# Performance work log

Measured on AMD Instinct MI355X. Metric: run time of the kernel, lower is better.

## Reference

```python
import jax, jax.numpy as jnp
import numpy as np

N_OSC = 32
CONV = 1000.0  # convergence_factor


def _cpg_ode(y, ia, ifr, cw, pb):
    # Faithful to CPGOde.forward, including its unpacking order:
    # (amplitudes, amplitudes_dot, phases) = (y[:n], y[n:2n], y[2n:3n])
    n = N_OSC
    a = y[:n]
    a_dot = y[n:2 * n]
    ph = y[2 * n:3 * n]
    phase_dots = ifr + jnp.sum(a[:, None] * cw * jnp.sin(ph[None, :] - ph[:, None] - pb), axis=1)
    a_dd = CONV * (CONV / 4.0 * (ia - a) - a_dot)
    # states_to_tensor(amplitudes_dot, phase_dots, amplitudes_dot_dot)
    return jnp.concatenate([a_dot, phase_dots, a_dd])


def _rk4_38_step(f, y, h):
    # torchdiffeq 'rk4' = rk4_alt_step_func (3/8 rule), one step over t=[0, h]
    k1 = f(y)
    k2 = f(y + h * k1 / 3.0)
    k3 = f(y + h * (k2 - k1 / 3.0))
    k4 = f(y + h * (k1 - k2 + k3))
    return y + h * 0.125 * (k1 + 3.0 * (k2 + k3) + k4)


def _mlp(x, Ws, bs):
    # Linear stack with ReLU between layers, none after the last
    for i, (W, b) in enumerate(zip(Ws, bs)):
        x = W @ x + b
        if i < len(Ws) - 1:
            x = jax.nn.relu(x)
    return x


def _init_linear(key, fan_in, fan_out):
    kW, kb = jax.random.split(key)
    bound = 1.0 / np.sqrt(fan_in)
    W = jax.random.uniform(kW, (fan_out, fan_in), minval=-bound, maxval=bound, dtype=jnp.float32)
    b = jax.random.uniform(kb, (fan_out,), minval=-bound, maxval=bound, dtype=jnp.float32)
    return W, b


def setup_inputs() -> dict:
    key = jax.random.key(0)
    ks = jax.random.split(key, 10)
    n = N_OSC
    n_params = 2 * n + 2 * n * n  # 2112
    in_dims = [2049, 4096, 4096, n_params]  # input_layers[0]+1, ..., final param layer
    out_dims = [2 * n, 2048, 2048, 1024]
    inp = {}
    inp["state"] = jax.random.normal(ks[0], (3 * n,), dtype=jnp.float32) * 0.1
    inp["x"] = jax.random.normal(ks[1], (2048,), dtype=jnp.float32)
    inp["timestep"] = jnp.array(0.01, dtype=jnp.float32)
    for i in range(3):
        W, b = _init_linear(ks[2 + i], in_dims[i], in_dims[i + 1])
        inp[f"in_W{i}"] = W
        inp[f"in_b{i}"] = b
    for i in range(3):
        W, b = _init_linear(ks[5 + i], out_dims[i], out_dims[i + 1])
        inp[f"out_W{i}"] = W
        inp[f"out_b{i}"] = b
    return inp


def reference(state, x, timestep,
              in_W0, in_b0, in_W1, in_b1, in_W2, in_b2,
              out_W0, out_b0, out_W1, out_b1, out_W2, out_b2):
    n = N_OSC
    # append timestep scalar to the input features
    x = jnp.concatenate([x, timestep[None]])
    params = _mlp(x, [in_W0, in_W1, in_W2], [in_b0, in_b1, in_b2])
    ia = params[:n]
    ifr = params[n:2 * n]
    cw = params[2 * n:2 * n + n * n].reshape(n, n)
    pb = params[2 * n + n * n:].reshape(n, n)
    f = lambda y: _cpg_ode(y, ia, ifr, cw, pb)
    new_state = _rk4_38_step(f, state, timestep)
    a = new_state[:n]
    ph = new_state[n:2 * n]
    cpg_out = jnp.concatenate([a * jnp.cos(ph), a * jnp.sin(ph)])
    out = _mlp(cpg_out, [out_W0, out_W1, out_W2], [out_b0, out_b1, out_b2])
    return (jax.lax.stop_gradient(new_state), out)
```

## Files before the change

kernel.cpp:

```cpp
#include <hip/hip_runtime.h>
#include <stdint.h>

template<int RELU, int TS>
__global__ __launch_bounds__(256) void gemv_k(
    const float* __restrict__ W, const float* __restrict__ B,
    const float* __restrict__ x, const float* __restrict__ ts,
    float* __restrict__ y, int cols)
{
    int tid = threadIdx.x;
    int row = blockIdx.x;
    int n = TS ? cols - 1 : cols;
    const float* w = W + (size_t)row * (size_t)cols;

    int mis = (int)(((uintptr_t)w >> 2) & 3);
    int start = (4 - mis) & 3;
    if (start > n) start = n;

    float sum = 0.0f;
    if (tid < start) sum += w[tid] * x[tid];

    int nv = (n - start) >> 2;
    const float4* wv = (const float4*)(w + start);
    const float* xs = x + start;

    int g = tid;
    for (; g + 768 < nv; g += 1024) {
        float4 u0 = wv[g];
        float4 u1 = wv[g + 256];
        float4 u2 = wv[g + 512];
        float4 u3 = wv[g + 768];
        const float* x0 = xs + 4 * g;
        const float* x1 = xs + 4 * (g + 256);
        const float* x2 = xs + 4 * (g + 512);
        const float* x3 = xs + 4 * (g + 768);
        sum += u0.x * x0[0] + u0.y * x0[1] + u0.z * x0[2] + u0.w * x0[3];
        sum += u1.x * x1[0] + u1.y * x1[1] + u1.z * x1[2] + u1.w * x1[3];
        sum += u2.x * x2[0] + u2.y * x2[1] + u2.z * x2[2] + u2.w * x2[3];
        sum += u3.x * x3[0] + u3.y * x3[1] + u3.z * x3[2] + u3.w * x3[3];
    }
    for (; g < nv; g += 256) {
        float4 u = wv[g];
        const float* xp = xs + 4 * g;
        sum += u.x * xp[0] + u.y * xp[1] + u.z * xp[2] + u.w * xp[3];
    }
    int t = start + nv * 4 + tid;
    if (t < n) sum += w[t] * x[t];
    if (TS && tid == 0) sum += w[n] * ts[0];

    #pragma unroll
    for (int off = 32; off > 0; off >>= 1) sum += __shfl_down(sum, off);
    __shared__ float red[4];
    if ((tid & 63) == 0) red[tid >> 6] = sum;
    __syncthreads();
    if (tid == 0) {
        float r = red[0] + red[1] + red[2] + red[3] + B[row];
        if (RELU) r = fmaxf(r, 0.0f);
        y[row] = r;
    }
}

__global__ __launch_bounds__(64) void ode_k(
    const float* __restrict__ state, const float* __restrict__ ts,
    const float* __restrict__ params, float* __restrict__ cpg,
    float* __restrict__ out_state)
{
    const float CONV = 1000.0f;
    __shared__ float s_cw[32 * 33];
    __shared__ float s_spb[32 * 33];
    __shared__ float s_cpb[32 * 33];
    __shared__ float s_s[32], s_c[32];
    int tid = threadIdx.x;

    for (int k = tid; k < 1024; k += 64) {
        int p = k + (k >> 5);
        s_cw[p] = params[64 + k];
        float pb = params[1088 + k];
        float sp, cp;
        sincosf(pb, &sp, &cp);
        s_spb[p] = sp;
        s_cpb[p] = cp;
    }
    __syncthreads();

    bool act = (tid < 32);
    int i = tid;
    float ia = 0.f, ifr = 0.f, y0a = 0.f, y0b = 0.f, y0c = 0.f;
    if (act) {
        ia  = params[i];
        ifr = params[32 + i];
        y0a = state[i];
        y0b = state[32 + i];
        y0c = state[64 + i];
    }
    float h = ts[0];

    float k1a=0,k1b=0,k1c=0, k2a=0,k2b=0,k2c=0, k3a=0,k3b=0,k3c=0, k4a=0,k4b=0,k4c=0;

    auto do_eval = [&](float a, float ad, float ph,
                       float& fa, float& fb, float& fc) {
        __syncthreads();
        if (act) {
            float s, c;
            sincosf(ph, &s, &c);
            s_s[i] = s; s_c[i] = c;
        }
        __syncthreads();
        if (act) {
            float si = s_s[i], ci = s_c[i];
            float ssum = 0.0f;
            #pragma unroll
            for (int j = 0; j < 32; j++) {
                float sj = s_s[j], cj = s_c[j];
                float sdp = sj * ci - cj * si;
                float cdp = cj * ci + sj * si;
                int p = i * 33 + j;
                float sv = sdp * s_cpb[p] - cdp * s_spb[p];
                ssum += s_cw[p] * sv;
            }
            fa = ad;
            fb = ifr + a * ssum;
            fc = CONV * (CONV * 0.25f * (ia - a) - ad);
        }
    };

    do_eval(y0a, y0b, y0c, k1a, k1b, k1c);
    do_eval(y0a + h * k1a / 3.0f,
            y0b + h * k1b / 3.0f,
            y0c + h * k1c / 3.0f, k2a, k2b, k2c);
    do_eval(y0a + h * (k2a - k1a / 3.0f),
            y0b + h * (k2b - k1b / 3.0f),
            y0c + h * (k2c - k1c / 3.0f), k3a, k3b, k3c);
    do_eval(y0a + h * (k1a - k2a + k3a),
            y0b + h * (k1b - k2b + k3b),
            y0c + h * (k1c - k2c + k3c), k4a, k4b, k4c);

    if (act) {
        float na = y0a + h * 0.125f * (k1a + 3.0f * (k2a + k3a) + k4a);
        float nb = y0b + h * 0.125f * (k1b + 3.0f * (k2b + k3b) + k4b);
        float nc = y0c + h * 0.125f * (k1c + 3.0f * (k2c + k3c) + k4c);
        out_state[i]      = na;
        out_state[32 + i] = nb;
        out_state[64 + i] = nc;
        cpg[i]      = na * cosf(nb);
        cpg[32 + i] = na * sinf(nb);
    }
}

extern "C" void kernel_launch(void* const* d_in, const int* in_sizes, int n_in,
                              void* d_out, int out_size, void* d_ws, size_t ws_size,
                              hipStream_t stream) {
    const float* state = (const float*)d_in[0];
    const float* x     = (const float*)d_in[1];
    const float* ts    = (const float*)d_in[2];
    const float* inW0  = (const float*)d_in[3];
    const float* inb0  = (const float*)d_in[4];
    const float* inW1  = (const float*)d_in[5];
    const float* inb1  = (const float*)d_in[6];
    const float* inW2  = (const float*)d_in[7];
    const float* inb2  = (const float*)d_in[8];
    const float* oW0   = (const float*)d_in[9];
    const float* ob0   = (const float*)d_in[10];
    const float* oW1   = (const float*)d_in[11];
    const float* ob1   = (const float*)d_in[12];
    const float* oW2   = (const float*)d_in[13];
    const float* ob2   = (const float*)d_in[14];

    float* ws  = (float*)d_ws;
    float* h0  = ws;
    float* h1  = ws + 4096;
    float* pr  = ws + 8192;
    float* cpg = ws + 10304;
    float* g0  = ws + 10368;
    float* g1  = ws + 12416;

    float* out = (float*)d_out;

    gemv_k<1,1><<<4096, 256, 0, stream>>>(inW0, inb0, x,   ts,      h0, 2049);
    gemv_k<1,0><<<4096, 256, 0, stream>>>(inW1, inb1, h0,  nullptr, h1, 4096);
    gemv_k<0,0><<<2112, 256, 0, stream>>>(inW2, inb2, h1,  nullptr, pr, 4096);
    ode_k<<<1, 64, 0, stream>>>(state, ts, pr, cpg, out);
    gemv_k<1,0><<<2048, 256, 0, stream>>>(oW0,  ob0,  cpg, nullptr, g0, 64);
    gemv_k<1,0><<<2048, 256, 0, stream>>>(oW1,  ob1,  g0,  nullptr, g1, 2048);
    gemv_k<0,0><<<1024, 256, 0, stream>>>(oW2,  ob2,  g1,  nullptr, out + 96, 2048);
}
```

Before: 214.1 us.

## Fuse all GEMV stages and ODE into one cooperative persistent kernel

Replaces the seven separate kernel launches with a single cooperative kernel of 1024 persistent blocks. Stages are separated by grid-wide syncs, and each block computes two rows per iteration. The ODE integrator now runs in block 0 with 256 threads. This removes launch gaps and tail idle between the small dependent stages, at the cost of grid.sync overhead, the loss of the 4-way unrolled load loop, and a fixed grid that may underfill the GPU during the bandwidth-bound large GEMVs.

```diff
diff --git a/kernel.cpp b/kernel.cpp
--- a/kernel.cpp
+++ b/kernel.cpp
@@ -1,82 +1,86 @@
 #include <hip/hip_runtime.h>
+#include <hip/hip_cooperative_groups.h>
 #include <stdint.h>
 
-template<int RELU, int TS>
-__global__ __launch_bounds__(256) void gemv_k(
-    const float* __restrict__ W, const float* __restrict__ B,
-    const float* __restrict__ x, const float* __restrict__ ts,
-    float* __restrict__ y, int cols)
-{
-    int tid = threadIdx.x;
-    int row = blockIdx.x;
-    int n = TS ? cols - 1 : cols;
-    const float* w = W + (size_t)row * (size_t)cols;
-
+namespace cg = cooperative_groups;
+
+#define NBLK 1024
+
+__device__ __forceinline__ float dot_row(const float* __restrict__ w,
+                                         const float* __restrict__ x,
+                                         int n, int tid)
+{
     int mis = (int)(((uintptr_t)w >> 2) & 3);
     int start = (4 - mis) & 3;
     if (start > n) start = n;
-
     float sum = 0.0f;
     if (tid < start) sum += w[tid] * x[tid];
-
     int nv = (n - start) >> 2;
     const float4* wv = (const float4*)(w + start);
     const float* xs = x + start;
-
-    int g = tid;
-    for (; g + 768 < nv; g += 1024) {
-        float4 u0 = wv[g];
-        float4 u1 = wv[g + 256];
-        float4 u2 = wv[g + 512];
-        float4 u3 = wv[g + 768];
-        const float* x0 = xs + 4 * g;
-        const float* x1 = xs + 4 * (g + 256);
-        const float* x2 = xs + 4 * (g + 512);
-        const float* x3 = xs + 4 * (g + 768);
-        sum += u0.x * x0[0] + u0.y * x0[1] + u0.z * x0[2] + u0.w * x0[3];
-        sum += u1.x * x1[0] + u1.y * x1[1] + u1.z * x1[2] + u1.w * x1[3];
-        sum += u2.x * x2[0] + u2.y * x2[1] + u2.z * x2[2] + u2.w * x2[3];
-        sum += u3.x * x3[0] + u3.y * x3[1] + u3.z * x3[2] + u3.w * x3[3];
-    }
-    for (; g < nv; g += 256) {
+    for (int g = tid; g < nv; g += 256) {
         float4 u = wv[g];
         const float* xp = xs + 4 * g;
         sum += u.x * xp[0] + u.y * xp[1] + u.z * xp[2] + u.w * xp[3];
     }
     int t = start + nv * 4 + tid;
     if (t < n) sum += w[t] * x[t];
-    if (TS && tid == 0) sum += w[n] * ts[0];
-
-    #pragma unroll
-    for (int off = 32; off > 0; off >>= 1) sum += __shfl_down(sum, off);
-    __shared__ float red[4];
-    if ((tid & 63) == 0) red[tid >> 6] = sum;
-    __syncthreads();
-    if (tid == 0) {
-        float r = red[0] + red[1] + red[2] + red[3] + B[row];
-        if (RELU) r = fmaxf(r, 0.0f);
-        y[row] = r;
-    }
-}
-
-__global__ __launch_bounds__(64) void ode_k(
-    const float* __restrict__ state, const float* __restrict__ ts,
-    const float* __restrict__ params, float* __restrict__ cpg,
-    float* __restrict__ out_state)
+    return sum;
+}
+
+template<int RELU, int TSCOL>
+__device__ void gemv_stage(const float* __restrict__ W, const float* __restrict__ B,
+                           const float* __restrict__ x, const float* __restrict__ ts,
+                           float* __restrict__ y, int rows, int cols,
+                           float* __restrict__ red)
+{
+    int tid = threadIdx.x;
+    int n = TSCOL ? cols - 1 : cols;
+    for (int base = blockIdx.x * 2; base < rows; base += NBLK * 2) {
+        int r1ok = (base + 1 < rows);
+        const float* w0 = W + (size_t)base * (size_t)cols;
+        const float* w1 = w0 + (r1ok ? cols : 0);
+        float s0 = dot_row(w0, x, n, tid);
+        float s1 = dot_row(w1, x, n, tid);
+        if (TSCOL && tid == 0) {
+            float t0 = ts[0];
+            s0 += w0[n] * t0;
+            s1 += w1[n] * t0;
+        }
+        #pragma unroll
+        for (int off = 32; off > 0; off >>= 1) {
+            s0 += __shfl_down(s0, off);
+            s1 += __shfl_down(s1, off);
+        }
+        __syncthreads();
+        if ((tid & 63) == 0) { red[tid >> 6] = s0; red[4 + (tid >> 6)] = s1; }
+        __syncthreads();
+        if (tid == 0) {
+            float r = red[0] + red[1] + red[2] + red[3] + B[base];
+            if (RELU) r = fmaxf(r, 0.0f);
+            y[base] = r;
+        } else if (tid == 64 && r1ok) {
+            float r = red[4] + red[5] + red[6] + red[7] + B[base + 1];
+            if (RELU) r = fmaxf(r, 0.0f);
+            y[base + 1] = r;
+        }
+    }
+}
+
+__device__ void ode_stage(const float* __restrict__ state, const float* __restrict__ ts,
+                          const float* __restrict__ params, float* __restrict__ cpg,
+                          float* __restrict__ out_state,
+                          float* s_cw, float* s_spb, float* s_cpb,
+                          float* s_s, float* s_c)
 {
     const float CONV = 1000.0f;
-    __shared__ float s_cw[32 * 33];
-    __shared__ float s_spb[32 * 33];
-    __shared__ float s_cpb[32 * 33];
-    __shared__ float s_s[32], s_c[32];
     int tid = threadIdx.x;
 
-    for (int k = tid; k < 1024; k += 64) {
+    for (int k = tid; k < 1024; k += 256) {
         int p = k + (k >> 5);
         s_cw[p] = params[64 + k];
-        float pb = params[1088 + k];
         float sp, cp;
-        sincosf(pb, &sp, &cp);
+        sincosf(params[1088 + k], &sp, &cp);
         s_spb[p] = sp;
         s_cpb[p] = cp;
     }
@@ -144,6 +148,45 @@
         cpg[i]      = na * cosf(nb);
         cpg[32 + i] = na * sinf(nb);
     }
+}
+
+__global__ __launch_bounds__(256, 4) void fused_k(
+    const float* state, const float* x, const float* ts,
+    const float* inW0, const float* inb0,
+    const float* inW1, const float* inb1,
+    const float* inW2, const float* inb2,
+    const float* oW0,  const float* ob0,
+    const float* oW1,  const float* ob1,
+    const float* oW2,  const float* ob2,
+    float* out, float* ws)
+{
+    cg::grid_group grid = cg::this_grid();
+
+    float* h0  = ws;
+    float* h1  = ws + 4096;
+    float* pr  = ws + 8192;
+    float* cpg = ws + 10304;
+    float* g0  = ws + 10368;
+    float* g1  = ws + 12416;
+
+    __shared__ float s_red[8];
+    __shared__ float s_cw[1056], s_spb[1056], s_cpb[1056];
+    __shared__ float s_s[32], s_c[32];
+
+    gemv_stage<1,1>(inW0, inb0, x,   ts, h0, 4096, 2049, s_red);
+    grid.sync();
+    gemv_stage<1,0>(inW1, inb1, h0,  nullptr, h1, 4096, 4096, s_red);
+    grid.sync();
+    gemv_stage<0,0>(inW2, inb2, h1,  nullptr, pr, 2112, 4096, s_red);
+    grid.sync();
+    if (blockIdx.x == 0)
+        ode_stage(state, ts, pr, cpg, out, s_cw, s_spb, s_cpb, s_s, s_c);
+    grid.sync();
+    gemv_stage<1,0>(oW0, ob0, cpg, nullptr, g0, 2048, 64, s_red);
+    grid.sync();
+    gemv_stage<1,0>(oW1, ob1, g0,  nullptr, g1, 2048, 2048, s_red);
+    grid.sync();
+    gemv_stage<0,0>(oW2, ob2, g1,  nullptr, out + 96, 1024, 2048, s_red);
 }
 
 extern "C" void kernel_launch(void* const* d_in, const int* in_sizes, int n_in,
@@ -165,21 +208,19 @@
     const float* oW2   = (const float*)d_in[13];
     const float* ob2   = (const float*)d_in[14];
 
+    float* out = (float*)d_out;
     float* ws  = (float*)d_ws;
-    float* h0  = ws;
-    float* h1  = ws + 4096;
-    float* pr  = ws + 8192;
-    float* cpg = ws + 10304;
-    float* g0  = ws + 10368;
-    float* g1  = ws + 12416;
-
-    float* out = (float*)d_out;
-
-    gemv_k<1,1><<<4096, 256, 0, stream>>>(inW0, inb0, x,   ts,      h0, 2049);
-    gemv_k<1,0><<<4096, 256, 0, stream>>>(inW1, inb1, h0,  nullptr, h1, 4096);
-    gemv_k<0,0><<<2112, 256, 0, stream>>>(inW2, inb2, h1,  nullptr, pr, 4096);
-    ode_k<<<1, 64, 0, stream>>>(state, ts, pr, cpg, out);
-    gemv_k<1,0><<<2048, 256, 0, stream>>>(oW0,  ob0,  cpg, nullptr, g0, 64);
-    gemv_k<1,0><<<2048, 256, 0, stream>>>(oW1,  ob1,  g0,  nullptr, g1, 2048);
-    gemv_k<0,0><<<1024, 256, 0, stream>>>(oW2,  ob2,  g1,  nullptr, out + 96, 2048);
-}
+
+    void* kargs[] = {
+        (void*)&state, (void*)&x, (void*)&ts,
+        (void*)&inW0, (void*)&inb0,
+        (void*)&inW1, (void*)&inb1,
+        (void*)&inW2, (void*)&inb2,
+        (void*)&oW0,  (void*)&ob0,
+        (void*)&oW1,  (void*)&ob1,
+        (void*)&oW2,  (void*)&ob2,
+        (void*)&out,  (void*)&ws
+    };
+    hipLaunchCooperativeKernel((const void*)fused_k, dim3(NBLK), dim3(256),
+                               kargs, 0, stream);
+}
```

After: 854.7 us. 299% more time.
